# Kernel tuning notes

Hardware: AMD Instinct MI355X
Metric: run time of the kernel (lower is better)

The kernel has to match this reference:

```python
import jax, jax.numpy as jnp
import numpy as np

N, E, F_IN, H, C = 50000, 800000, 64, 4, 32
NEG_SLOPE = 0.2  # PyG GATConv default negative_slope
LN_EPS = 1e-5


def setup_inputs() -> dict:
    key = jax.random.key(0)
    ks = jax.random.split(key, 8)
    s = 1.0 / np.sqrt(F_IN)
    return {
        "x": jax.random.normal(ks[0], (N, F_IN), jnp.float32),
        "edge_index": jax.random.randint(ks[1], (2, E), 0, N, jnp.int64),
        "W": jax.random.normal(ks[2], (F_IN, H * C), jnp.float32) * s,
        "att_src": jax.random.normal(ks[3], (H, C), jnp.float32) * s,
        "att_dst": jax.random.normal(ks[4], (H, C), jnp.float32) * s,
        "bias": jnp.zeros((H * C,), jnp.float32),
        "res_w": jax.random.normal(ks[5], (F_IN, H * C), jnp.float32) * s,
        "res_b": jnp.zeros((H * C,), jnp.float32),
        "ln_g": jnp.ones((H * C,), jnp.float32),
        "ln_b": jnp.zeros((H * C,), jnp.float32),
    }


def reference(x, edge_index, W, att_src, att_dst, bias, res_w, res_b, ln_g, ln_b):
    n = x.shape[0]
    # GATConv adds self-loops by default
    loop = jnp.arange(n, dtype=edge_index.dtype)
    src = jnp.concatenate([edge_index[0], loop])
    dst = jnp.concatenate([edge_index[1], loop])

    h = (x @ W).reshape(n, H, C)                      # [N,H,C]
    a_src = jnp.einsum('nhc,hc->nh', h, att_src)       # [N,H]
    a_dst = jnp.einsum('nhc,hc->nh', h, att_dst)

    e = a_src[src] + a_dst[dst]                        # [Etot,H]
    e = jnp.where(e >= 0, e, NEG_SLOPE * e)            # leaky_relu

    # segment softmax over destination nodes
    m = jax.ops.segment_max(e, dst, num_segments=n)    # [N,H]
    ex = jnp.exp(e - m[dst])
    denom = jax.ops.segment_sum(ex, dst, num_segments=n)
    alpha = ex / denom[dst]                            # [Etot,H]

    msg = h[src] * alpha[:, :, None]                   # [Etot,H,C]
    out = jax.ops.segment_sum(msg, dst, num_segments=n)  # [N,H,C]
    out = out.reshape(n, H * C) + bias

    # elu; dropout is identity in eval mode
    out = jnp.where(out > 0, out, jnp.expm1(out))
    out = out + (x @ res_w + res_b)                    # residual Linear

    mu = out.mean(-1, keepdims=True)
    var = ((out - mu) ** 2).mean(-1, keepdims=True)
    return ln_g * (out - mu) * jax.lax.rsqrt(var + LN_EPS) + ln_b
```

## Files before the change

### kernel.cpp

```cpp
#include <hip/hip_runtime.h>

#define F_IN 64
#define NH 4
#define HC 128
#define NEG_SLOPE 0.2f
#define LN_EPS 1e-5f
#define BUCKET 128
#define BKT_CAP 2560
#define NSC 128
#define CCAP 44
#define KREG 25

typedef __bf16 bf16_8 __attribute__((ext_vector_type(8)));
typedef float  f32_4  __attribute__((ext_vector_type(4)));

__device__ inline int detect_is64(const int* __restrict__ ei, int E) {
    int lane = threadIdx.x & 63;
    long long stride = (2LL * E) / 65;
    int w = ei[(((long long)(lane + 1)) * stride) | 1];
    return __ballot(w != 0) == 0ULL;
}

__device__ inline unsigned bfpack(float a, float b) {
    unsigned ua = __float_as_uint(a), ub = __float_as_uint(b);
    ua = (ua + 0x7fffu + ((ua >> 16) & 1u)) >> 16;
    ub = (ub + 0x7fffu + ((ub >> 16) & 1u)) >> 16;
    return ua | (ub << 16);
}

__global__ __launch_bounds__(256) void k_main(
    const float* __restrict__ x, const float* __restrict__ W,
    const float* __restrict__ res_w,
    const float* __restrict__ att_src, const float* __restrict__ att_dst,
    __bf16* __restrict__ wt,
    unsigned* __restrict__ h_bf, unsigned* __restrict__ r_bf,
    float* __restrict__ a_s, float* __restrict__ a_d, int n,
    const int* __restrict__ ei, int E,
    int* __restrict__ counts, unsigned* __restrict__ epk, int chunk, int NB)
{
    __shared__ int bcur[512];

    if ((int)blockIdx.x >= NSC) {
        int tid = threadIdx.x;
#pragma unroll
        for (int jj = 0; jj < 32; ++jj) {
            int idx = jj * 256 + tid;
            int ch = idx >> 5;
            int j5 = idx & 31;
            int k0 = j5 * 2;
            const float* src = (ch < HC) ? W : res_w;
            int cc = ch & (HC - 1);
            float lo = src[k0 * HC + cc];
            float hi = src[(k0 + 1) * HC + cc];
            ((unsigned*)wt)[ch * 32 + j5] = bfpack(lo, hi);
        }
        __syncthreads();

        int wv_ = tid >> 6, lane = tid & 63;
        int col = lane & 15, quad = lane >> 4;
        int node = (blockIdx.x - NSC) * 64 + wv_ * 16 + col;
        int nrow = (node < n) ? node : (n - 1);

        bf16_8 bx0, bx1;
        {
            const float* xp = &x[nrow * F_IN + quad * 8];
            float4 p0 = *(const float4*)(xp);
            float4 p1 = *(const float4*)(xp + 4);
            float4 p2 = *(const float4*)(xp + 32);
            float4 p3 = *(const float4*)(xp + 36);
            bx0[0] = (__bf16)p0.x; bx0[1] = (__bf16)p0.y; bx0[2] = (__bf16)p0.z; bx0[3] = (__bf16)p0.w;
            bx0[4] = (__bf16)p1.x; bx0[5] = (__bf16)p1.y; bx0[6] = (__bf16)p1.z; bx0[7] = (__bf16)p1.w;
            bx1[0] = (__bf16)p2.x; bx1[1] = (__bf16)p2.y; bx1[2] = (__bf16)p2.z; bx1[3] = (__bf16)p2.w;
            bx1[4] = (__bf16)p3.x; bx1[5] = (__bf16)p3.y; bx1[6] = (__bf16)p3.z; bx1[7] = (__bf16)p3.w;
        }

        float vs[4] = {0.f, 0.f, 0.f, 0.f};
        float vd[4] = {0.f, 0.f, 0.f, 0.f};

#pragma unroll
        for (int mt = 0; mt < 16; ++mt) {
            const __bf16* ap = &wt[(mt * 16 + col) * 64 + quad * 8];
            bf16_8 a0 = *(const bf16_8*)ap;
            bf16_8 a1 = *(const bf16_8*)(ap + 32);
            f32_4 acc = {0.f, 0.f, 0.f, 0.f};
            acc = __builtin_amdgcn_mfma_f32_16x16x32_bf16(a0, bx0, acc, 0, 0, 0);
            acc = __builtin_amdgcn_mfma_f32_16x16x32_bf16(a1, bx1, acc, 0, 0, 0);
            int ch0 = mt * 16 + quad * 4;
            if (mt < 8) {
                float4 as4 = *(const float4*)&att_src[ch0];
                float4 ad4 = *(const float4*)&att_dst[ch0];
                int head = mt >> 1;
                vs[head] += acc[0] * as4.x + acc[1] * as4.y + acc[2] * as4.z + acc[3] * as4.w;
                vd[head] += acc[0] * ad4.x + acc[1] * ad4.y + acc[2] * ad4.z + acc[3] * ad4.w;
                if (node < n) {
                    uint2 pk = make_uint2(bfpack(acc[0], acc[1]), bfpack(acc[2], acc[3]));
                    *(uint2*)&h_bf[node * 64 + (ch0 >> 1)] = pk;
                }
            } else {
                if (node < n) {
                    uint2 pk = make_uint2(bfpack(acc[0], acc[1]), bfpack(acc[2], acc[3]));
                    *(uint2*)&r_bf[node * 64 + ((ch0 - 128) >> 1)] = pk;
                }
            }
        }

#pragma unroll
        for (int hh = 0; hh < NH; ++hh) {
            vs[hh] += __shfl_down(vs[hh], 32, 64);
            vs[hh] += __shfl_down(vs[hh], 16, 64);
            vd[hh] += __shfl_down(vd[hh], 32, 64);
            vd[hh] += __shfl_down(vd[hh], 16, 64);
        }
        if (quad == 0 && node < n) {
            *(float4*)&a_s[node * NH] = make_float4(vs[0], vs[1], vs[2], vs[3]);
            *(float4*)&a_d[node * NH] = make_float4(vd[0], vd[1], vd[2], vd[3]);
        }
        return;
    }

    int c = blockIdx.x, t = threadIdx.x;
    for (int i = t; i < NB; i += 256) bcur[i] = 0;
    __syncthreads();
    int is64 = detect_is64(ei, E);
    int base = c * chunk, end = min(E, base + chunk);

    unsigned rg[KREG];
#pragma unroll
    for (int i = 0; i < KREG; ++i) {
        int idx = base + i * 256 + t;
        unsigned ent = 0xFFFFFFFFu;
        if (idx < end) {
            int s = is64 ? ei[2 * idx] : ei[idx];
            int d = is64 ? ei[2 * (E + idx)] : ei[E + idx];
            ent = ((unsigned)d << 16) | (unsigned)s;
            atomicAdd(&bcur[d >> 7], 1);
        }
        rg[i] = ent;
    }
    __syncthreads();

    for (int bb = t; bb < NB; bb += 256) {
        int f = bcur[bb]; if (f > CCAP) f = CCAP;
        counts[c * NB + bb] = f;
        bcur[bb] = 0;
    }
    __syncthreads();

#pragma unroll
    for (int i = 0; i < KREG; ++i) {
        unsigned ent = rg[i];
        if (ent != 0xFFFFFFFFu) {
            int bb = ent >> 23;
            int p = atomicAdd(&bcur[bb], 1);
            if (p < CCAP)
                epk[((size_t)c * NB + bb) * CCAP + p] = ent;
        }
    }
}

__global__ __launch_bounds__(256) void kd_sort(
    const int* __restrict__ counts, const unsigned* __restrict__ epk,
    unsigned short* __restrict__ ssorted, unsigned* __restrict__ offdeg,
    int n, int NB)
{
    __shared__ int cnt_s[NSC];
    __shared__ int hist[BUCKET], sc[BUCKET], cur[BUCKET];
    int b = blockIdx.x, t = threadIdx.x;
    if (t < NSC) cnt_s[t] = counts[t * NB + b];
    if (t < BUCKET) hist[t] = 0;
    __syncthreads();

    for (int slot = t; slot < NSC * CCAP; slot += 256) {
        int c = slot / CCAP, j = slot - c * CCAP;
        if (j < cnt_s[c]) {
            unsigned ent = epk[((size_t)c * NB + b) * CCAP + j];
            atomicAdd(&hist[(ent >> 16) & (BUCKET - 1)], 1);
        }
    }
    __syncthreads();

    if (t < BUCKET) sc[t] = (hist[t] + 1) & ~1;
    __syncthreads();
#pragma unroll
    for (int o = 1; o < BUCKET; o <<= 1) {
        int u = (t >= o && t < BUCKET) ? sc[t - o] : 0;
        __syncthreads();
        if (t < BUCKET) sc[t] += u;
        __syncthreads();
    }
    if (t < BUCKET) {
        int excl = sc[t] - ((hist[t] + 1) & ~1);
        cur[t] = excl;
        int d = b * BUCKET + t;
        if (d < n)
            offdeg[d] = ((unsigned)(b * BKT_CAP + excl) << 12) | (unsigned)hist[t];
    }
    __syncthreads();

    unsigned short* outp = ssorted + (size_t)b * BKT_CAP;
    for (int slot = t; slot < NSC * CCAP; slot += 256) {
        int c = slot / CCAP, j = slot - c * CCAP;
        if (j < cnt_s[c]) {
            unsigned ent = epk[((size_t)c * NB + b) * CCAP + j];
            int p = atomicAdd(&cur[(ent >> 16) & (BUCKET - 1)], 1);
            if (p < BKT_CAP) outp[p] = (unsigned short)(ent & 0xffffu);
        }
    }
}

__global__ __launch_bounds__(256) void k_agg(
    const unsigned* __restrict__ offdeg, const unsigned short* __restrict__ ssorted,
    const float* __restrict__ a_s, const float* __restrict__ a_d,
    const unsigned int* __restrict__ h_bf, const unsigned int* __restrict__ r_bf,
    const float* __restrict__ bias, const float* __restrict__ res_b,
    const float* __restrict__ ln_g, const float* __restrict__ ln_b,
    float* __restrict__ out, int n)
{
    int wv = threadIdx.x >> 6, lane = threadIdx.x & 63;
    int d = blockIdx.x * 4 + wv;
    if (d >= n) return;
    int eh = lane >> 4;
    int g  = lane & 15;
    int head = g >> 2;
    float ad = a_d[d * NH + head];

    float ac[8] = {0.f, 0.f, 0.f, 0.f, 0.f, 0.f, 0.f, 0.f};
    float denom = 0.f;

#define ACCUM(WW, VV)                                                      \
    do {                                                                   \
        ac[0] += (WW) * __uint_as_float((VV).x << 16);                     \
        ac[1] += (WW) * __uint_as_float((VV).x & 0xffff0000u);             \
        ac[2] += (WW) * __uint_as_float((VV).y << 16);                     \
        ac[3] += (WW) * __uint_as_float((VV).y & 0xffff0000u);             \
        ac[4] += (WW) * __uint_as_float((VV).z << 16);                     \
        ac[5] += (WW) * __uint_as_float((VV).z & 0xffff0000u);             \
        ac[6] += (WW) * __uint_as_float((VV).w << 16);                     \
        ac[7] += (WW) * __uint_as_float((VV).w & 0xffff0000u);             \
    } while (0)

    {
        float e = a_s[d * NH + head] + ad;
        e = fmaxf(e, NEG_SLOPE * e);
        float w = (eh == 0) ? __expf(e) : 0.f;
        uint4 hv = *(const uint4*)&h_bf[d * 64 + 4 * g];
        ACCUM(w, hv);
        denom += w;
    }

    unsigned od = offdeg[d];
    int deg = od & 4095;
    const unsigned short* sl = &ssorted[od >> 12];
    int k = 0;
    if (k + 7 < deg) {
        unsigned sp = *(const unsigned*)&sl[k + 2 * eh];
        for (; k + 7 < deg; ) {
            int kn = k + 8;
            unsigned spn = 0;
            if (kn + 7 < deg)
                spn = *(const unsigned*)&sl[kn + 2 * eh];
            int s0 = sp & 0xffffu, s1 = sp >> 16;
            float e0 = a_s[s0 * NH + head];
            float e1 = a_s[s1 * NH + head];
            uint4 v0 = *(const uint4*)&h_bf[s0 * 64 + 4 * g];
            uint4 v1 = *(const uint4*)&h_bf[s1 * 64 + 4 * g];
            e0 += ad; e0 = fmaxf(e0, NEG_SLOPE * e0);
            float w0 = __expf(e0);
            e1 += ad; e1 = fmaxf(e1, NEG_SLOPE * e1);
            float w1 = __expf(e1);
            denom += w0 + w1;
            ACCUM(w0, v0);
            ACCUM(w1, v1);
            sp = spn; k = kn;
        }
    }
    for (; k < deg; k += 4) {
        int idx = k + eh;
        int valid = idx < deg;
        int s0 = valid ? sl[idx] : 0;
        float e0 = a_s[s0 * NH + head] + ad;
        uint4 v0 = *(const uint4*)&h_bf[s0 * 64 + 4 * g];
        e0 = fmaxf(e0, NEG_SLOPE * e0);
        float w0 = valid ? __expf(e0) : 0.f;
        denom += w0;
        ACCUM(w0, v0);
    }
#undef ACCUM

#pragma unroll
    for (int j = 0; j < 8; ++j) {
        ac[j] += __shfl_xor(ac[j], 32, 64);
        ac[j] += __shfl_xor(ac[j], 16, 64);
    }
    denom += __shfl_xor(denom, 32, 64);
    denom += __shfl_xor(denom, 16, 64);

    int c0 = g * 8;
    float4 bi0 = *(const float4*)&bias[c0];
    float4 bi1 = *(const float4*)&bias[c0 + 4];
    float4 rb0 = *(const float4*)&res_b[c0];
    float4 rb1 = *(const float4*)&res_b[c0 + 4];
    uint4 rv = *(const uint4*)&r_bf[d * 64 + 4 * g];

    float inv = 1.f / denom;
    float o[8];
    o[0] = ac[0] * inv + bi0.x; o[1] = ac[1] * inv + bi0.y;
    o[2] = ac[2] * inv + bi0.z; o[3] = ac[3] * inv + bi0.w;
    o[4] = ac[4] * inv + bi1.x; o[5] = ac[5] * inv + bi1.y;
    o[6] = ac[6] * inv + bi1.z; o[7] = ac[7] * inv + bi1.w;
#pragma unroll
    for (int j = 0; j < 8; ++j)
        o[j] = (o[j] > 0.f) ? o[j] : (__expf(o[j]) - 1.f);
    o[0] += __uint_as_float(rv.x << 16) + rb0.x;
    o[1] += __uint_as_float(rv.x & 0xffff0000u) + rb0.y;
    o[2] += __uint_as_float(rv.y << 16) + rb0.z;
    o[3] += __uint_as_float(rv.y & 0xffff0000u) + rb0.w;
    o[4] += __uint_as_float(rv.z << 16) + rb1.x;
    o[5] += __uint_as_float(rv.z & 0xffff0000u) + rb1.y;
    o[6] += __uint_as_float(rv.w << 16) + rb1.z;
    o[7] += __uint_as_float(rv.w & 0xffff0000u) + rb1.w;

    float ps = o[0] + o[1] + o[2] + o[3] + o[4] + o[5] + o[6] + o[7];
#pragma unroll
    for (int off = 32; off > 0; off >>= 1) ps += __shfl_down(ps, off, 64);
    float mean = __shfl(ps, 0, 64) * (1.f / (4 * HC));
    float dv[8], pv = 0.f;
#pragma unroll
    for (int j = 0; j < 8; ++j) { dv[j] = o[j] - mean; pv += dv[j] * dv[j]; }
#pragma unroll
    for (int off = 32; off > 0; off >>= 1) pv += __shfl_down(pv, off, 64);
    float var = __shfl(pv, 0, 64) * (1.f / (4 * HC));
    float rs = rsqrtf(var + LN_EPS);
    if (eh == 0) {
        float4 gg0 = *(const float4*)&ln_g[c0];
        float4 gg1 = *(const float4*)&ln_g[c0 + 4];
        float4 lb0 = *(const float4*)&ln_b[c0];
        float4 lb1 = *(const float4*)&ln_b[c0 + 4];
        *(float4*)&out[d * HC + c0] =
            make_float4(gg0.x * dv[0] * rs + lb0.x, gg0.y * dv[1] * rs + lb0.y,
                        gg0.z * dv[2] * rs + lb0.z, gg0.w * dv[3] * rs + lb0.w);
        *(float4*)&out[d * HC + c0 + 4] =
            make_float4(gg1.x * dv[4] * rs + lb1.x, gg1.y * dv[5] * rs + lb1.y,
                        gg1.z * dv[6] * rs + lb1.z, gg1.w * dv[7] * rs + lb1.w);
    }
}

extern "C" void kernel_launch(void* const* d_in, const int* in_sizes, int n_in,
                              void* d_out, int out_size, void* d_ws, size_t ws_size,
                              hipStream_t stream) {
    const float* x       = (const float*)d_in[0];
    const int*   ei      = (const int*)d_in[1];
    const float* W       = (const float*)d_in[2];
    const float* att_src = (const float*)d_in[3];
    const float* att_dst = (const float*)d_in[4];
    const float* bias    = (const float*)d_in[5];
    const float* res_w   = (const float*)d_in[6];
    const float* res_b   = (const float*)d_in[7];
    const float* ln_g    = (const float*)d_in[8];
    const float* ln_b    = (const float*)d_in[9];
    float* out = (float*)d_out;

    int n = in_sizes[0] / F_IN;
    int E = in_sizes[1] / 2;
    int NB = (n + BUCKET - 1) / BUCKET;
    int chunk = (E + NSC - 1) / NSC;
    int nka = (n + 63) / 64;

    unsigned*       h_bf   = (unsigned*)d_ws;
    unsigned*       r_bf   = h_bf + (size_t)n * 64;
    float*          a_s    = (float*)(r_bf + (size_t)n * 64);
    float*          a_d    = a_s + (size_t)n * NH;
    int*            counts = (int*)(a_d + (size_t)n * NH);
    unsigned*       epk    = (unsigned*)(counts + NSC * NB);
    unsigned short* ssd    = (unsigned short*)(epk + (size_t)NSC * NB * CCAP);
    unsigned*       offdeg = (unsigned*)(ssd + (size_t)NB * BKT_CAP);
    __bf16*         wt     = (__bf16*)(offdeg + n);

    k_main<<<NSC + nka, 256, 0, stream>>>(
        x, W, res_w, att_src, att_dst, wt, h_bf, r_bf, a_s, a_d, n,
        ei, E, counts, epk, chunk, NB);

    kd_sort<<<NB, 256, 0, stream>>>(counts, epk, ssd, offdeg, n, NB);

    k_agg<<<(n + 3) / 4, 256, 0, stream>>>(offdeg, ssd, a_s, a_d, h_bf, r_bf,
                                           bias, res_b, ln_g, ln_b, out, n);
}
```

Measured before the change: 193.1 us.

## Stage transposed bf16 weights in padded LDS and software-pipeline aggregation gathers

The GEMM blocks now convert W and res_w into a padded shared-memory tile (row stride 72) instead of writing a transposed bf16 copy to global workspace and reading it back. This removes a global round-trip and fixes a latent race, since before each block wrote the global wt buffer and then read it after only a block-level barrier. The aggregation inner loop is software-pipelined so the next pair of neighbor indices, attention scalars and feature vectors is loaded before the current pair is accumulated, hiding gather latency. The trade-off is 36KB of LDS per block, which may lower occupancy for the scatter blocks that share the kernel, plus extra registers for the prefetched values.

Result: faster. 162.7 us (-15.8%).

```diff
diff --git a/kernel.cpp b/kernel.cpp
--- a/kernel.cpp
+++ b/kernel.cpp
@@ -10,6 +10,7 @@
 #define NSC 128
 #define CCAP 44
 #define KREG 25
+#define WT_LD 72
 
 typedef __bf16 bf16_8 __attribute__((ext_vector_type(8)));
 typedef float  f32_4  __attribute__((ext_vector_type(4)));
@@ -32,27 +33,23 @@
     const float* __restrict__ x, const float* __restrict__ W,
     const float* __restrict__ res_w,
     const float* __restrict__ att_src, const float* __restrict__ att_dst,
-    __bf16* __restrict__ wt,
     unsigned* __restrict__ h_bf, unsigned* __restrict__ r_bf,
     float* __restrict__ a_s, float* __restrict__ a_d, int n,
     const int* __restrict__ ei, int E,
     int* __restrict__ counts, unsigned* __restrict__ epk, int chunk, int NB)
 {
-    __shared__ int bcur[512];
+    __shared__ __align__(16) char smem[256 * WT_LD * 2];
 
     if ((int)blockIdx.x >= NSC) {
+        __bf16* wtl = (__bf16*)smem;
         int tid = threadIdx.x;
-#pragma unroll
-        for (int jj = 0; jj < 32; ++jj) {
-            int idx = jj * 256 + tid;
-            int ch = idx >> 5;
-            int j5 = idx & 31;
-            int k0 = j5 * 2;
-            const float* src = (ch < HC) ? W : res_w;
-            int cc = ch & (HC - 1);
-            float lo = src[k0 * HC + cc];
-            float hi = src[(k0 + 1) * HC + cc];
-            ((unsigned*)wt)[ch * 32 + j5] = bfpack(lo, hi);
+        for (int it = 0; it < 64; ++it) {
+            int idx = it * 256 + tid;
+            const float* src = (idx < 8192) ? W : res_w;
+            int off = idx & 8191;
+            int k = off >> 7, cc = off & 127;
+            int ch = ((idx >> 13) << 7) | cc;
+            wtl[ch * WT_LD + k] = (__bf16)src[off];
         }
         __syncthreads();
 
@@ -79,7 +76,7 @@
 
 #pragma unroll
         for (int mt = 0; mt < 16; ++mt) {
-            const __bf16* ap = &wt[(mt * 16 + col) * 64 + quad * 8];
+            const __bf16* ap = &wtl[(mt * 16 + col) * WT_LD + quad * 8];
             bf16_8 a0 = *(const bf16_8*)ap;
             bf16_8 a1 = *(const bf16_8*)(ap + 32);
             f32_4 acc = {0.f, 0.f, 0.f, 0.f};
@@ -118,6 +115,7 @@
         return;
     }
 
+    int* bcur = (int*)smem;
     int c = blockIdx.x, t = threadIdx.x;
     for (int i = t; i < NB; i += 256) bcur[i] = 0;
     __syncthreads();
@@ -253,25 +251,35 @@
     const unsigned short* sl = &ssorted[od >> 12];
     int k = 0;
     if (k + 7 < deg) {
-        unsigned sp = *(const unsigned*)&sl[k + 2 * eh];
-        for (; k + 7 < deg; ) {
+        unsigned sp = *(const unsigned*)&sl[2 * eh];
+        int s0 = sp & 0xffffu, s1 = sp >> 16;
+        float e0 = a_s[s0 * NH + head];
+        float e1 = a_s[s1 * NH + head];
+        uint4 v0 = *(const uint4*)&h_bf[s0 * 64 + 4 * g];
+        uint4 v1 = *(const uint4*)&h_bf[s1 * 64 + 4 * g];
+        while (true) {
             int kn = k + 8;
-            unsigned spn = 0;
-            if (kn + 7 < deg)
-                spn = *(const unsigned*)&sl[kn + 2 * eh];
-            int s0 = sp & 0xffffu, s1 = sp >> 16;
-            float e0 = a_s[s0 * NH + head];
-            float e1 = a_s[s1 * NH + head];
-            uint4 v0 = *(const uint4*)&h_bf[s0 * 64 + 4 * g];
-            uint4 v1 = *(const uint4*)&h_bf[s1 * 64 + 4 * g];
-            e0 += ad; e0 = fmaxf(e0, NEG_SLOPE * e0);
-            float w0 = __expf(e0);
-            e1 += ad; e1 = fmaxf(e1, NEG_SLOPE * e1);
-            float w1 = __expf(e1);
+            int more = (kn + 7 < deg);
+            float ne0 = 0.f, ne1 = 0.f;
+            uint4 nv0 = {0u,0u,0u,0u}, nv1 = {0u,0u,0u,0u};
+            if (more) {
+                unsigned spn = *(const unsigned*)&sl[kn + 2 * eh];
+                int t0 = spn & 0xffffu, t1 = spn >> 16;
+                ne0 = a_s[t0 * NH + head];
+                ne1 = a_s[t1 * NH + head];
+                nv0 = *(const uint4*)&h_bf[t0 * 64 + 4 * g];
+                nv1 = *(const uint4*)&h_bf[t1 * 64 + 4 * g];
+            }
+            float f0 = e0 + ad; f0 = fmaxf(f0, NEG_SLOPE * f0);
+            float w0 = __expf(f0);
+            float f1 = e1 + ad; f1 = fmaxf(f1, NEG_SLOPE * f1);
+            float w1 = __expf(f1);
             denom += w0 + w1;
             ACCUM(w0, v0);
             ACCUM(w1, v1);
-            sp = spn; k = kn;
+            k = kn;
+            if (!more) break;
+            e0 = ne0; e1 = ne1; v0 = nv0; v1 = nv1;
         }
     }
     for (; k < deg; k += 4) {
@@ -374,10 +382,9 @@
     unsigned*       epk    = (unsigned*)(counts + NSC * NB);
     unsigned short* ssd    = (unsigned short*)(epk + (size_t)NSC * NB * CCAP);
     unsigned*       offdeg = (unsigned*)(ssd + (size_t)NB * BKT_CAP);
-    __bf16*         wt     = (__bf16*)(offdeg + n);
 
     k_main<<<NSC + nka, 256, 0, stream>>>(
-        x, W, res_w, att_src, att_dst, wt, h_bf, r_bf, a_s, a_d, n,
+        x, W, res_w, att_src, att_dst, h_bf, r_bf, a_s, a_d, n,
         ei, E, counts, epk, chunk, NB);
 
     kd_sort<<<NB, 256, 0, stream>>>(counts, epk, ssd, offdeg, n, NB);
```
